# Performance work log

Hardware: AMD Instinct MI355X
Metric: run time of the kernel (lower is better)

The kernel has to match this reference:

```python
import jax, jax.numpy as jnp
import numpy as np

B, C, L = 32, 64, 4096
HIDDEN = 64
SR = 50.0
KS = (7, 15, 31, 63)
PHYS = 12
EPS_BN = 1e-5
EPS_GN = 1e-5


def _dwconv(x, w):
    # x: (B,C,L), w: (C,1,k) depthwise kernel, SAME padding for odd k
    k = w.shape[-1]
    p = (k - 1) // 2
    return jax.lax.conv_general_dilated(
        x, w, window_strides=(1,), padding=[(p, p)],
        dimension_numbers=('NCH', 'OIH', 'NCH'),
        feature_group_count=x.shape[1])


def _physics(x):
    b, c, l = x.shape
    svm = jnp.sqrt((x * x).sum(axis=1))                      # (B,L) channel norm
    svm_max = svm.max(axis=-1)
    svm_mean = svm.mean(axis=-1)
    svm_std = jnp.std(svm, axis=-1, ddof=1) + 1e-6           # torch.std is unbiased
    jerk = jnp.diff(x, axis=-1) * SR                         # (B,C,L-1)
    jerk_max = jnp.abs(jerk).max(axis=-1).mean(axis=-1)      # (B,)
    jerk_rate = jnp.diff(jerk, axis=-1) * SR
    jerk_rate_max = jnp.abs(jerk_rate).max(axis=-1).mean(axis=-1)
    sign_changes = (x[:, :, :-1] * x[:, :, 1:] < 0).astype(x.dtype)
    zcr = sign_changes.sum(axis=-1).mean(axis=-1) / l
    thr = (svm_mean + 2.0 * svm_std)[:, None]
    impact_duration = (svm > thr).astype(x.dtype).sum(axis=-1) / l
    hthr = (svm_mean + 3.0 * svm_std)[:, None]
    impact_ratio = (svm > hthr).astype(x.dtype).sum(axis=-1) / l
    free_fall = (svm < (svm_mean - svm_std)[:, None]).astype(x.dtype).sum(axis=-1) / l
    second_half = svm[:, l // 2:]
    post_stillness = jnp.tanh(1.0 / (jnp.std(second_half, axis=-1, ddof=1) + 1e-6))
    third = max(1, l // 3)
    pre_mean = svm[:, :third].mean(axis=-1)
    impact_peak = svm[:, third:2 * third].max(axis=-1)
    post_mean = svm[:, 2 * third:].mean(axis=-1)
    fall_phase = jax.nn.relu(impact_peak - pre_mean) + jax.nn.relu(impact_peak - post_mean)
    fall_phase = fall_phase / (jnp.abs(impact_peak) + 1e-6)
    spectrum = jnp.fft.rfft(x.astype(jnp.float32), axis=-1, norm='ortho')
    power = (jnp.abs(spectrum) ** 2).sum(axis=1)             # (B, L//2+1)
    freqs = jnp.linspace(0.0, 1.0, power.shape[-1], dtype=power.dtype)
    total_power = power.sum(axis=-1) + 1e-6
    spectral_centroid = (power * freqs).sum(axis=-1) / total_power
    high_freq_ratio = jnp.where(freqs > 0.4, power, 0.0).sum(axis=-1) / total_power
    feats = jnp.stack([svm_max, svm_mean, jerk_max, jerk_rate_max, zcr,
                       impact_duration, impact_ratio, post_stillness, free_fall,
                       spectral_centroid, high_freq_ratio, fall_phase], axis=-1)
    return jnp.nan_to_num(feats, nan=0.0, posinf=0.0, neginf=0.0).astype(x.dtype)


def _forward(x, dw_w7, dw_w15, dw_w31, dw_w63, bn_g, bn_b, bn_m, bn_v,
             comp_w1, comp_b1, comp_w2, comp_b2,
             pn_g, pn_b, pn_m, pn_v,
             pe_w1, pe_b1, pe_w2, pe_b2, pg_w, pg_b,
             temperature, gn_g, gn_b, proj_w, proj_b, res_scale):
    # 4 depthwise conv + BN(eval) branches
    branches = []
    for i, w in enumerate((dw_w7, dw_w15, dw_w31, dw_w63)):
        y = _dwconv(x, w)
        y = (y - bn_m[i][None, :, None]) / jnp.sqrt(bn_v[i][None, :, None] + EPS_BN) \
            * bn_g[i][None, :, None] + bn_b[i][None, :, None]
        branches.append(y)
    stacked = jnp.stack(branches, axis=1)                    # (B,4,C,L)
    # complexity net: global avg pool -> MLP
    xm = x.mean(axis=-1)                                     # (B,C)
    h = jax.nn.relu(xm @ comp_w1 + comp_b1)
    complexity_logits = h @ comp_w2 + comp_b2                # (B,4)
    # physics gate
    pf = _physics(x)                                         # (B,12)
    pf = (pf - pn_m) / jnp.sqrt(pn_v + EPS_BN) * pn_g + pn_b
    pe = jax.nn.relu(jax.nn.relu(pf @ pe_w1 + pe_b1) @ pe_w2 + pe_b2)
    physics_weights = jax.nn.sigmoid(pe @ pg_w + pg_b)       # (B,4)
    temp = jnp.maximum(temperature, 0.1)
    weights = jax.nn.softmax(complexity_logits * physics_weights / temp, axis=-1)
    mixed = jnp.einsum('bkcl,bk->bcl', stacked, weights)
    # proj: GroupNorm(1,C) -> GELU(exact) -> 1x1 conv
    mu = mixed.mean(axis=(1, 2), keepdims=True)
    var = mixed.var(axis=(1, 2), keepdims=True)
    gn = (mixed - mu) / jnp.sqrt(var + EPS_GN) * gn_g[None, :, None] + gn_b[None, :, None]
    act = jax.nn.gelu(gn, approximate=False)
    out = jnp.einsum('oc,bcl->bol', proj_w, act) + proj_b[None, :, None]
    return x + res_scale * out


def setup_inputs() -> dict:
    ks = jax.random.split(jax.random.key(0), 16)
    f32 = jnp.float32
    inp = {}
    inp['x'] = jax.random.normal(ks[0], (B, C, L), dtype=f32)
    for i, k in enumerate(KS):
        inp[f'dw_w{k}'] = jax.random.normal(ks[1 + i], (C, 1, k), dtype=f32) / np.sqrt(k)
    inp['bn_g'] = jnp.ones((4, C), f32)
    inp['bn_b'] = jnp.zeros((4, C), f32)
    inp['bn_m'] = 0.1 * jax.random.normal(ks[5], (4, C), dtype=f32)
    inp['bn_v'] = jax.random.uniform(ks[6], (4, C), dtype=f32, minval=0.5, maxval=1.5)
    inp['comp_w1'] = jax.random.normal(ks[7], (C, HIDDEN), dtype=f32) / np.sqrt(C)
    inp['comp_b1'] = jnp.zeros((HIDDEN,), f32)
    inp['comp_w2'] = jax.random.normal(ks[8], (HIDDEN, 4), dtype=f32) / np.sqrt(HIDDEN)
    inp['comp_b2'] = jnp.zeros((4,), f32)
    inp['pn_g'] = jnp.ones((PHYS,), f32)
    inp['pn_b'] = jnp.zeros((PHYS,), f32)
    inp['pn_m'] = 0.1 * jax.random.normal(ks[9], (PHYS,), dtype=f32)
    inp['pn_v'] = jax.random.uniform(ks[10], (PHYS,), dtype=f32, minval=0.5, maxval=1.5)
    inp['pe_w1'] = jax.random.normal(ks[11], (PHYS, 32), dtype=f32) / np.sqrt(PHYS)
    inp['pe_b1'] = jnp.zeros((32,), f32)
    inp['pe_w2'] = jax.random.normal(ks[12], (32, 32), dtype=f32) / np.sqrt(32)
    inp['pe_b2'] = jnp.zeros((32,), f32)
    inp['pg_w'] = jax.random.normal(ks[13], (32, 4), dtype=f32) / np.sqrt(32)
    inp['pg_b'] = jnp.zeros((4,), f32)
    inp['temperature'] = jnp.asarray(1.0, f32)
    inp['gn_g'] = jnp.ones((C,), f32)
    inp['gn_b'] = jnp.zeros((C,), f32)
    inp['proj_w'] = jax.random.normal(ks[14], (C, C), dtype=f32) / np.sqrt(C)
    inp['proj_b'] = jnp.zeros((C,), f32)
    inp['res_scale'] = jnp.asarray(0.5, f32)  # init is 0.0; 0.5 gives a non-trivial output
    return inp


def reference(x, dw_w7, dw_w15, dw_w31, dw_w63, bn_g, bn_b, bn_m, bn_v,
              comp_w1, comp_b1, comp_w2, comp_b2,
              pn_g, pn_b, pn_m, pn_v,
              pe_w1, pe_b1, pe_w2, pe_b2, pg_w, pg_b,
              temperature, gn_g, gn_b, proj_w, proj_b, res_scale):
    return _forward(x, dw_w7, dw_w15, dw_w31, dw_w63, bn_g, bn_b, bn_m, bn_v,
                    comp_w1, comp_b1, comp_w2, comp_b2, pn_g, pn_b, pn_m, pn_v,
                    pe_w1, pe_b1, pe_w2, pe_b2, pg_w, pg_b,
                    temperature, gn_g, gn_b, proj_w, proj_b, res_scale)
```

## Files before the change

kernel.cpp:

```cpp
#include <hip/hip_runtime.h>
#include <math.h>

#define LN 4096
#define CN 64
#define NTH 256

#define OFF_CHAN_SUM    0
#define OFF_CHAN_JERK   2048
#define OFF_CHAN_JRATE  4096
#define OFF_CHAN_ZCR    6144
#define OFF_SVMST_PART  8192
#define OFF_SPEC_PART   16384
#define OFF_GNP         19584
#define OFF_SVMBUF      27776

#define FP(i) ((i) + ((i) >> 4))

__device__ __forceinline__ void bfly4(float2& a, float2& b, float2& c, float2& d,
                                      float w1r, float w1i, float w2r, float w2i,
                                      float w3r, float w3i) {
  float t1r = b.x*w1r - b.y*w1i, t1i = b.x*w1i + b.y*w1r;
  float t2r = c.x*w2r - c.y*w2i, t2i = c.x*w2i + c.y*w2r;
  float t3r = d.x*w3r - d.y*w3i, t3i = d.x*w3i + d.y*w3r;
  float ar = a.x + t2r, ai = a.y + t2i;
  float br = a.x - t2r, bi = a.y - t2i;
  float cr = t1r + t3r, ci = t1i + t3i;
  float dr = t1r - t3r, di = t1i - t3i;
  a = make_float2(ar + cr, ai + ci);
  b = make_float2(br + di, bi - dr);
  c = make_float2(ar - cr, ai - ci);
  d = make_float2(br - di, bi + dr);
}

__device__ __forceinline__ float4 ldmask(const float* __restrict__ row, int idx) {
  int idxc = idx < 0 ? 0 : (idx > LN - 4 ? LN - 4 : idx);
  float4 v = *(const float4*)(row + idxc);
  float m = (idx == idxc) ? 1.f : 0.f;
  v.x *= m; v.y *= m; v.z *= m; v.w *= m;
  return v;
}

#define F16(wv,a0,a1,a2,a3,a4,a5,a6,a7,a8,a9,aA,aB,aC,aD,aE,aF) \
  acc[0]=fmaf(wv,a0,acc[0]);  acc[1]=fmaf(wv,a1,acc[1]);  acc[2]=fmaf(wv,a2,acc[2]);  acc[3]=fmaf(wv,a3,acc[3]);  \
  acc[4]=fmaf(wv,a4,acc[4]);  acc[5]=fmaf(wv,a5,acc[5]);  acc[6]=fmaf(wv,a6,acc[6]);  acc[7]=fmaf(wv,a7,acc[7]);  \
  acc[8]=fmaf(wv,a8,acc[8]);  acc[9]=fmaf(wv,a9,acc[9]);  acc[10]=fmaf(wv,aA,acc[10]); acc[11]=fmaf(wv,aB,acc[11]); \
  acc[12]=fmaf(wv,aC,acc[12]); acc[13]=fmaf(wv,aD,acc[13]); acc[14]=fmaf(wv,aE,acc[14]); acc[15]=fmaf(wv,aF,acc[15]);

__global__ __launch_bounds__(NTH) void k1_spec(const float* __restrict__ x, float* __restrict__ ws) {
  __shared__ __align__(16) char smraw[35072];
  int i = blockIdx.x;
  int b = i >> 5, sl = i & 31;
  int t = threadIdx.x;

  {
    float* tmp = (float*)smraw;
    float (*sred)[8] = (float(*)[8])(smraw + 512);
    int lt = t & 127, ch = t >> 7;
    int l = sl * 128 + lt;
    const float* xb = x + (size_t)b * CN * LN + l;
    float acc = 0.f;
#pragma unroll
    for (int cc = 0; cc < 32; cc++) {
      float v = xb[(size_t)(ch * 32 + cc) * LN];
      acc = fmaf(v, v, acc);
    }
    if (ch == 1) tmp[lt] = acc;
    __syncthreads();
    if (ch == 0) {
      acc += tmp[lt];
      float svm = sqrtf(acc);
      ws[OFF_SVMBUF + (size_t)b * LN + l] = svm;
      const int third = LN / 3;
      float vS = svm, vS2 = svm * svm;
      float vS2H  = (l >= LN/2) ? svm : 0.f;
      float vS2H2 = (l >= LN/2) ? svm * svm : 0.f;
      float vPRE  = (l < third) ? svm : 0.f;
      float vPOST = (l >= 2*third) ? svm : 0.f;
      float vMX = svm;
      float vMID = (l >= third && l < 2*third) ? svm : 0.f;
      for (int off = 32; off > 0; off >>= 1) {
        vS += __shfl_down(vS, off); vS2 += __shfl_down(vS2, off);
        vS2H += __shfl_down(vS2H, off); vS2H2 += __shfl_down(vS2H2, off);
        vPRE += __shfl_down(vPRE, off); vPOST += __shfl_down(vPOST, off);
        vMX = fmaxf(vMX, __shfl_down(vMX, off));
        vMID = fmaxf(vMID, __shfl_down(vMID, off));
      }
      if ((t & 63) == 0) {
        int w = t >> 6;
        sred[w][0]=vS; sred[w][1]=vS2; sred[w][2]=vMX; sred[w][3]=vS2H;
        sred[w][4]=vS2H2; sred[w][5]=vPRE; sred[w][6]=vMID; sred[w][7]=vPOST;
      }
    }
    __syncthreads();
    if (t == 0) {
      float* sp = ws + OFF_SVMST_PART + (size_t)(b * 32 + sl) * 8;
      sp[0]=sred[0][0]+sred[1][0];
      sp[1]=sred[0][1]+sred[1][1];
      sp[2]=fmaxf(sred[0][2],sred[1][2]);
      sp[3]=sred[0][3]+sred[1][3];
      sp[4]=sred[0][4]+sred[1][4];
      sp[5]=sred[0][5]+sred[1][5];
      sp[6]=fmaxf(sred[0][6],sred[1][6]);
      sp[7]=sred[0][7]+sred[1][7];
    }
    __syncthreads();
  }

  {
    const float* r0 = x + ((size_t)b * CN + 2 * sl) * LN;
    const float* r1 = r0 + LN;
    float2* z = (float2*)smraw;
    float (*sred8)[8] = (float(*)[8])(smraw + 34816);
    float s0 = 0.f, jm0 = 0.f, jr0 = 0.f; int zc0 = 0;
    float s1v = 0.f, jm1 = 0.f, jr1 = 0.f; int zc1 = 0;
#pragma unroll
    for (int k = 0; k < 4; k++) {
      int n4 = (k * 256 + t) * 4;
      float4 a = *(const float4*)(r0 + n4);
      float4 c = *(const float4*)(r1 + n4);
      float a4 = __shfl_down(a.x, 1), a5 = __shfl_down(a.y, 1);
      float c4 = __shfl_down(c.x, 1), c5 = __shfl_down(c.y, 1);
      if ((t & 63) == 63) {
        a4 = (n4 + 4 < LN) ? r0[n4 + 4] : 0.f;
        a5 = (n4 + 5 < LN) ? r0[n4 + 5] : 0.f;
        c4 = (n4 + 4 < LN) ? r1[n4 + 4] : 0.f;
        c5 = (n4 + 5 < LN) ? r1[n4 + 5] : 0.f;
      }
      bool nl = (n4 + 4 < LN);
      s0 += a.x + a.y + a.z + a.w;
      jm0 = fmaxf(jm0, fmaxf(fmaxf(fabsf(a.y-a.x), fabsf(a.z-a.y)), fabsf(a.w-a.z)));
      zc0 += (a.x*a.y < 0.f) + (a.y*a.z < 0.f) + (a.z*a.w < 0.f);
      jr0 = fmaxf(jr0, fmaxf(fabsf(a.z - 2.f*a.y + a.x), fabsf(a.w - 2.f*a.z + a.y)));
      if (nl) {
        jm0 = fmaxf(jm0, fabsf(a4 - a.w));
        zc0 += (a.w * a4 < 0.f);
        jr0 = fmaxf(jr0, fmaxf(fabsf(a4 - 2.f*a.w + a.z), fabsf(a5 - 2.f*a4 + a.w)));
      }
      s1v += c.x + c.y + c.z + c.w;
      jm1 = fmaxf(jm1, fmaxf(fmaxf(fabsf(c.y-c.x), fabsf(c.z-c.y)), fabsf(c.w-c.z)));
      zc1 += (c.x*c.y < 0.f) + (c.y*c.z < 0.f) + (c.z*c.w < 0.f);
      jr1 = fmaxf(jr1, fmaxf(fabsf(c.z - 2.f*c.y + c.x), fabsf(c.w - 2.f*c.z + c.y)));
      if (nl) {
        jm1 = fmaxf(jm1, fabsf(c4 - c.w));
        zc1 += (c.w * c4 < 0.f);
        jr1 = fmaxf(jr1, fmaxf(fabsf(c4 - 2.f*c.w + c.z), fabsf(c5 - 2.f*c4 + c.w)));
      }
      float ar[4] = {a.x, a.y, a.z, a.w}, crr[4] = {c.x, c.y, c.z, c.w};
#pragma unroll
      for (int q = 0; q < 4; q++) {
        unsigned n = (unsigned)(n4 + q);
        unsigned br = __brev(n) >> 20;
        unsigned dr = ((br & 0x555u) << 1) | ((br & 0xAAAu) >> 1);
        z[FP(dr)] = make_float2(ar[q], crr[q]);
      }
    }
    for (int off = 32; off > 0; off >>= 1) {
      s0 += __shfl_down(s0, off); jm0 = fmaxf(jm0, __shfl_down(jm0, off));
      jr0 = fmaxf(jr0, __shfl_down(jr0, off)); zc0 += __shfl_down(zc0, off);
      s1v += __shfl_down(s1v, off); jm1 = fmaxf(jm1, __shfl_down(jm1, off));
      jr1 = fmaxf(jr1, __shfl_down(jr1, off)); zc1 += __shfl_down(zc1, off);
    }
    if ((t & 63) == 0) {
      int w = t >> 6;
      sred8[w][0]=s0; sred8[w][1]=jm0; sred8[w][2]=jr0; sred8[w][3]=(float)zc0;
      sred8[w][4]=s1v; sred8[w][5]=jm1; sred8[w][6]=jr1; sred8[w][7]=(float)zc1;
    }
    __syncthreads();
    if (t == 0) {
      int bc0 = b * CN + 2 * sl;
      float S0=0,J0=0,JR0=0,Z0=0,S1=0,J1=0,JR1=0,Z1=0;
      for (int w = 0; w < 4; w++) {
        S0 += sred8[w][0]; J0 = fmaxf(J0, sred8[w][1]); JR0 = fmaxf(JR0, sred8[w][2]); Z0 += sred8[w][3];
        S1 += sred8[w][4]; J1 = fmaxf(J1, sred8[w][5]); JR1 = fmaxf(JR1, sred8[w][6]); Z1 += sred8[w][7];
      }
      ws[OFF_CHAN_SUM + bc0]       = S0;           ws[OFF_CHAN_SUM + bc0 + 1]   = S1;
      ws[OFF_CHAN_JERK + bc0]      = J0 * 50.f;    ws[OFF_CHAN_JERK + bc0 + 1]  = J1 * 50.f;
      ws[OFF_CHAN_JRATE + bc0]     = JR0 * 2500.f; ws[OFF_CHAN_JRATE + bc0 + 1] = JR1 * 2500.f;
      ws[OFF_CHAN_ZCR + bc0]       = Z0;           ws[OFF_CHAN_ZCR + bc0 + 1]   = Z1;
    }
    const float c8r[4] = { 1.f, 0.92387953251f, 0.70710678119f, 0.38268343236f };
    const float c8i[4] = { 0.f, -0.38268343236f, -0.70710678119f, -0.92387953251f };
#pragma unroll
    for (int p = 0; p < 3; p++) {
      const int H = (p == 0) ? 1 : (p == 1) ? 16 : 256;
      int rr = t & (H - 1);
      int B = ((t / H) * 16 * H) + rr;
      float2 E[16];
#pragma unroll
      for (int q = 0; q < 16; q++) E[q] = z[FP(B + q * H)];
      float su, cu;
      sincospif((float)rr / (8.0f * (float)H), &su, &cu);
      float ur = cu, ui = -su;
      float u2r = ur*ur - ui*ui, u2i = 2.f*ur*ui;
      float w1r = u2r*u2r - u2i*u2i, w1i = 2.f*u2r*u2i;
      float w2r = w1r*w1r - w1i*w1i, w2i = 2.f*w1r*w1i;
      float w3r = w2r*w1r - w2i*w1i, w3i = w2r*w1i + w2i*w1r;
#pragma unroll
      for (int m = 0; m < 4; m++)
        bfly4(E[4*m], E[4*m+1], E[4*m+2], E[4*m+3], w1r, w1i, w2r, w2i, w3r, w3i);
#pragma unroll
      for (int m = 0; m < 4; m++) {
        float W1r = ur*c8r[m] - ui*c8i[m];
        float W1i = ur*c8i[m] + ui*c8r[m];
        float W2r = W1r*W1r - W1i*W1i, W2i = 2.f*W1r*W1i;
        float W3r = W2r*W1r - W2i*W1i, W3i = W2r*W1i + W2i*W1r;
        bfly4(E[m], E[m+4], E[m+8], E[m+12], W1r, W1i, W2r, W2i, W3r, W3i);
      }
#pragma unroll
      for (int q = 0; q < 16; q++) z[FP(B + q * H)] = E[q];
      __syncthreads();
    }
    float tot = 0.f, cen = 0.f, hi = 0.f;
    for (int k = t; k <= LN / 2; k += NTH) {
      float p;
      if (k == 0 || k == LN / 2) {
        float2 v = z[FP(k)];
        p = v.x * v.x + v.y * v.y;
      } else {
        float2 zk = z[FP(k)], zn = z[FP(LN - k)];
        float a1 = zk.x + zn.x, a2 = zk.y - zn.y, a3 = zk.y + zn.y, a4v = zk.x - zn.x;
        p = 0.25f * (a1*a1 + a2*a2 + a3*a3 + a4v*a4v);
      }
      p *= (1.0f / LN);
      tot += p;
      cen += p * ((float)k * (1.0f / (LN / 2)));
      if (k >= 820) hi += p;
    }
    for (int off = 32; off > 0; off >>= 1) {
      tot += __shfl_down(tot, off);
      cen += __shfl_down(cen, off);
      hi  += __shfl_down(hi, off);
    }
    float (*redS)[4] = (float(*)[4])(smraw + 34816);
    if ((t & 63) == 0) { int w = t >> 6; redS[0][w] = tot; redS[1][w] = cen; redS[2][w] = hi; }
    __syncthreads();
    if (t == 0) {
      float* sp = ws + OFF_SPEC_PART + (size_t)(b * 32 + sl) * 3;
      sp[0] = redS[0][0]+redS[0][1]+redS[0][2]+redS[0][3];
      sp[1] = redS[1][0]+redS[1][1]+redS[1][2]+redS[1][3];
      sp[2] = redS[2][0]+redS[2][1]+redS[2][2]+redS[2][3];
    }
  }
}

__global__ __launch_bounds__(NTH) void k2_conv(
    const float* __restrict__ x,
    const float* __restrict__ dw7, const float* __restrict__ dw15,
    const float* __restrict__ dw31, const float* __restrict__ dw63,
    const float* __restrict__ bn_g, const float* __restrict__ bn_b,
    const float* __restrict__ bn_m, const float* __restrict__ bn_v,
    const float* __restrict__ comp_w1, const float* __restrict__ comp_b1,
    const float* __restrict__ comp_w2, const float* __restrict__ comp_b2,
    const float* __restrict__ pn_g, const float* __restrict__ pn_b,
    const float* __restrict__ pn_m, const float* __restrict__ pn_v,
    const float* __restrict__ pe_w1, const float* __restrict__ pe_b1,
    const float* __restrict__ pe_w2, const float* __restrict__ pe_b2,
    const float* __restrict__ pg_w, const float* __restrict__ pg_b,
    const float* __restrict__ temperature,
    float* __restrict__ ws, float* __restrict__ out)
{
  int i = blockIdx.x;
  int b = i >> 5, sl = i & 31;
  int t = threadIdx.x;
  __shared__ float sp8[32][8];
  __shared__ float sp3[32][3];
  __shared__ float stv[10];
  __shared__ float bc2[2];
  __shared__ float xm[64], h[64], pf[12], pe1v[32], pe2v[32], lgts[4], swts[4];
  __shared__ int ri[3][4], cnts[3];
  __shared__ float cwt[2][64];
  __shared__ float cbias[2];
  __shared__ double rda[2][4];

  if (t < 32) {
    const float* p = ws + OFF_SVMST_PART + (size_t)(b * 32 + t) * 8;
#pragma unroll
    for (int q = 0; q < 8; q++) sp8[t][q] = p[q];
  }
  if (t >= 32 && t < 64) {
    int q = t - 32;
    const float* p = ws + OFF_SPEC_PART + (size_t)(b * 32 + q) * 3;
    sp3[q][0] = p[0]; sp3[q][1] = p[1]; sp3[q][2] = p[2];
  }
  __syncthreads();
  if (t == 0) {
    float S=0,S2=0,MX=-1e30f,S2H=0,S2H2=0,PRE=0,MID=-1e30f,POST=0;
    for (int q = 0; q < 32; q++) {
      S += sp8[q][0]; S2 += sp8[q][1]; MX = fmaxf(MX, sp8[q][2]);
      S2H += sp8[q][3]; S2H2 += sp8[q][4]; PRE += sp8[q][5];
      MID = fmaxf(MID, sp8[q][6]); POST += sp8[q][7];
    }
    float tt=0,ce=0,hh=0;
    for (int q = 0; q < 32; q++) { tt += sp3[q][0]; ce += sp3[q][1]; hh += sp3[q][2]; }
    stv[0]=S; stv[1]=S2; stv[2]=MX; stv[3]=S2H; stv[4]=S2H2;
    stv[5]=PRE; stv[6]=MID; stv[7]=POST; stv[8]=ce/(tt+1e-6f); stv[9]=hh/(tt+1e-6f);
    float mean = S * (1.f / LN);
    float var = (S2 - S * S * (1.f / LN)) * (1.f / (LN - 1));
    var = fmaxf(var, 0.f);
    bc2[0] = mean;
    bc2[1] = sqrtf(var) + 1e-6f;
  }
  __syncthreads();
  float mean = bc2[0], stde = bc2[1];
  float thr2 = mean + 2.f * stde, thr3 = mean + 3.f * stde, thrf = mean - stde;
  const float* svm = ws + OFF_SVMBUF + (size_t)b * LN;
  int cc2 = 0, cc3 = 0, ccf = 0;
  for (int l = t; l < LN; l += NTH) {
    float v = svm[l];
    cc2 += (v > thr2); cc3 += (v > thr3); ccf += (v < thrf);
  }
  for (int off = 32; off > 0; off >>= 1) {
    cc2 += __shfl_down(cc2, off); cc3 += __shfl_down(cc3, off); ccf += __shfl_down(ccf, off);
  }
  {
    int w = t >> 6;
    if ((t & 63) == 0) { ri[0][w] = cc2; ri[1][w] = cc3; ri[2][w] = ccf; }
  }
  float j = 0.f, jr = 0.f, zz = 0.f;
  if (t < 64) {
    xm[t] = ws[OFF_CHAN_SUM + b * 64 + t] * (1.0f / LN);
    j  = ws[OFF_CHAN_JERK + b * 64 + t];
    jr = ws[OFF_CHAN_JRATE + b * 64 + t];
    zz = ws[OFF_CHAN_ZCR + b * 64 + t];
    for (int off = 32; off > 0; off >>= 1) {
      j += __shfl_down(j, off); jr += __shfl_down(jr, off); zz += __shfl_down(zz, off);
    }
  }
  __syncthreads();
  if (t == 0) {
    cnts[0] = ri[0][0]+ri[0][1]+ri[0][2]+ri[0][3];
    cnts[1] = ri[1][0]+ri[1][1]+ri[1][2]+ri[1][3];
    cnts[2] = ri[2][0]+ri[2][1]+ri[2][2]+ri[2][3];
    const int third = LN / 3;
    float S2H = stv[3], S2H2 = stv[4];
    float n2 = (float)(LN / 2);
    float var2 = (S2H2 - S2H * S2H / n2) / (n2 - 1.f);
    var2 = fmaxf(var2, 0.f);
    float post_still = tanhf(1.f / (sqrtf(var2) + 1e-6f));
    float pre_mean = stv[5] / (float)third;
    float post_mean = stv[7] / (float)(LN - 2 * third);
    float pk = stv[6];
    float fp2 = fmaxf(pk - pre_mean, 0.f) + fmaxf(pk - post_mean, 0.f);
    fp2 = fp2 / (fabsf(pk) + 1e-6f);
    pf[0] = stv[2];
    pf[1] = mean;
    pf[2] = j * (1.f / 64);
    pf[3] = jr * (1.f / 64);
    pf[4] = (zz * (1.f / 64)) * (1.f / LN);
    pf[5] = (float)cnts[0] / LN;
    pf[6] = (float)cnts[1] / LN;
    pf[7] = post_still;
    pf[8] = (float)cnts[2] / LN;
    pf[9] = stv[8];
    pf[10] = stv[9];
    pf[11] = fp2;
  }
  __syncthreads();
  if (t < 12) pf[t] = (pf[t] - pn_m[t]) * rsqrtf(pn_v[t] + 1e-5f) * pn_g[t] + pn_b[t];
  __syncthreads();
  if (t < 64) {
    float hv = comp_b1[t];
    for (int q = 0; q < 64; q++) hv = fmaf(xm[q], comp_w1[q * 64 + t], hv);
    h[t] = fmaxf(hv, 0.f);
  }
  if (t < 32) {
    float v = pe_b1[t];
    for (int q = 0; q < 12; q++) v = fmaf(pf[q], pe_w1[q * 32 + t], v);
    pe1v[t] = fmaxf(v, 0.f);
  }
  __syncthreads();
  if (t < 32) {
    float v = pe_b2[t];
    for (int q = 0; q < 32; q++) v = fmaf(pe1v[q], pe_w2[q * 32 + t], v);
    pe2v[t] = fmaxf(v, 0.f);
  }
  __syncthreads();
  if (t < 4) {
    float v = comp_b2[t];
    for (int q = 0; q < 64; q++) v = fmaf(h[q], comp_w2[q * 4 + t], v);
    float g = pg_b[t];
    for (int q = 0; q < 32; q++) g = fmaf(pe2v[q], pg_w[q * 4 + t], g);
    g = 1.f / (1.f + expf(-g));
    float temp = fmaxf(temperature[0], 0.1f);
    lgts[t] = v * g / temp;
  }
  __syncthreads();
  if (t < 4) {
    float m = fmaxf(fmaxf(lgts[0], lgts[1]), fmaxf(lgts[2], lgts[3]));
    float den = expf(lgts[0]-m) + expf(lgts[1]-m) + expf(lgts[2]-m) + expf(lgts[3]-m);
    swts[t] = expf(lgts[t] - m) / den;
  }
  __syncthreads();

  if (t < 128) {
    int rr = t >> 6, tau = t & 63;
    int c = 2 * sl + rr;
    float w0 = swts[0], w1 = swts[1], w2 = swts[2], w3 = swts[3];
    float sc0 = bn_g[0*64+c] * rsqrtf(bn_v[0*64+c] + 1e-5f);
    float sc1 = bn_g[1*64+c] * rsqrtf(bn_v[1*64+c] + 1e-5f);
    float sc2 = bn_g[2*64+c] * rsqrtf(bn_v[2*64+c] + 1e-5f);
    float sc3 = bn_g[3*64+c] * rsqrtf(bn_v[3*64+c] + 1e-5f);
    float a0 = w0*sc0, a1 = w1*sc1, a2 = w2*sc2, a3 = w3*sc3;
    if (tau == 0) {
      float o0 = bn_b[0*64+c] - bn_m[0*64+c] * sc0;
      float o1 = bn_b[1*64+c] - bn_m[1*64+c] * sc1;
      float o2 = bn_b[2*64+c] - bn_m[2*64+c] * sc2;
      float o3 = bn_b[3*64+c] - bn_m[3*64+c] * sc3;
      cbias[rr] = w0*o0 + w1*o1 + w2*o2 + w3*o3;
    }
    float v = 0.f;
    if (tau < 63) {
      v = a3 * dw63[c * 63 + tau];
      int i7 = tau - 28;  if (i7 >= 0 && i7 < 7)    v = fmaf(a0, dw7[c * 7 + i7], v);
      int i15 = tau - 24; if (i15 >= 0 && i15 < 15) v = fmaf(a1, dw15[c * 15 + i15], v);
      int i31 = tau - 16; if (i31 >= 0 && i31 < 31) v = fmaf(a2, dw31[c * 31 + i31], v);
    }
    cwt[rr][tau] = v;
  }
  __syncthreads();

#pragma unroll 1
  for (int r = 0; r < 2; r++) {
    int c = 2 * sl + r;
    const float* row = x + ((size_t)b * CN + c) * LN;
    const float* wtp = cwt[r];
    float bias = cbias[r];
    int l0 = t * 16, g0 = l0 - 32;
    float4 R0 = ldmask(row, g0);
    float4 R1 = ldmask(row, g0 + 4);
    float4 R2 = ldmask(row, g0 + 8);
    float4 R3 = ldmask(row, g0 + 12);
    float4 R4 = ldmask(row, g0 + 16);
    float acc[16];
#pragma unroll
    for (int jj = 0; jj < 16; jj++) acc[jj] = bias;
#pragma unroll
    for (int g = 0; g < 16; g++) {
      float w0 = wtp[4*g], w1 = wtp[4*g+1], w2 = wtp[4*g+2], w3 = wtp[4*g+3];
      F16(w0, R0.y,R0.z,R0.w,R1.x,R1.y,R1.z,R1.w,R2.x,R2.y,R2.z,R2.w,R3.x,R3.y,R3.z,R3.w,R4.x)
      F16(w1, R0.z,R0.w,R1.x,R1.y,R1.z,R1.w,R2.x,R2.y,R2.z,R2.w,R3.x,R3.y,R3.z,R3.w,R4.x,R4.y)
      F16(w2, R0.w,R1.x,R1.y,R1.z,R1.w,R2.x,R2.y,R2.z,R2.w,R3.x,R3.y,R3.z,R3.w,R4.x,R4.y,R4.z)
      F16(w3, R1.x,R1.y,R1.z,R1.w,R2.x,R2.y,R2.z,R2.w,R3.x,R3.y,R3.z,R3.w,R4.x,R4.y,R4.z,R4.w)
      if (g < 15) {
        R0 = R1; R1 = R2; R2 = R3; R3 = R4;
        R4 = ldmask(row, g0 + 4 * (g + 5));
      }
    }
    double ls = 0, ls2 = 0;
#pragma unroll
    for (int jj = 0; jj < 16; jj++) { float v = acc[jj]; ls += v; ls2 += (double)v * (double)v; }
    for (int off = 32; off > 0; off >>= 1) {
      ls += __shfl_down(ls, off);
      ls2 += __shfl_down(ls2, off);
    }
    int w = t >> 6;
    if ((t & 63) == 0) { rda[0][w] = ls; rda[1][w] = ls2; }
    float* dst = out + (size_t)(b * CN + c) * LN + l0;
#pragma unroll
    for (int q = 0; q < 4; q++) {
      float4 v4; v4.x = acc[4*q]; v4.y = acc[4*q+1]; v4.z = acc[4*q+2]; v4.w = acc[4*q+3];
      *(float4*)(dst + 4 * q) = v4;
    }
    __syncthreads();
    if (t == 0) {
      double* gp = (double*)(ws + OFF_GNP);
      gp[2 * (b * CN + c) + 0] = rda[0][0]+rda[0][1]+rda[0][2]+rda[0][3];
      gp[2 * (b * CN + c) + 1] = rda[1][0]+rda[1][1]+rda[1][2]+rda[1][3];
    }
    __syncthreads();
  }
}

__global__ __launch_bounds__(NTH) void k3_final(const float* __restrict__ x,
    const float* __restrict__ proj_w, const float* __restrict__ proj_b,
    const float* __restrict__ gn_g, const float* __restrict__ gn_b,
    const float* __restrict__ res_scale,
    const float* __restrict__ ws, float* out) {
  __shared__ __align__(16) char smraw[32840];
  int i = blockIdx.x;
  int b = i >> 5, sl = i & 31;
  int t = threadIdx.x;
  float* Wt   = (float*)smraw;
  float* actS = (float*)(smraw + 16384);
  double (*rg)[4] = (double(*)[4])(smraw + 32768);
  float* bcst = (float*)(smraw + 32832);
  const double* gp = (const double*)(ws + OFF_GNP) + (size_t)b * CN * 2;
  double g1 = 0, g2 = 0;
  if (t < CN) { g1 = gp[2*t]; g2 = gp[2*t+1]; }
  for (int off = 32; off > 0; off >>= 1) { g1 += __shfl_down(g1, off); g2 += __shfl_down(g2, off); }
  {
    int w = t >> 6;
    if ((t & 63) == 0) { rg[0][w] = g1; rg[1][w] = g2; }
  }
  for (int q = t; q < 4096; q += NTH) {
    int o = q & 63, c = q >> 6;
    Wt[c * 64 + o] = proj_w[o * 64 + c];
  }
  __syncthreads();
  if (t == 0) {
    double S1 = rg[0][0]+rg[0][1]+rg[0][2]+rg[0][3];
    double S2 = rg[1][0]+rg[1][1]+rg[1][2]+rg[1][3];
    const double NN = 64.0 * 4096.0;
    double mud = S1 / NN;
    bcst[0] = (float)mud;
    bcst[1] = rsqrtf((float)(S2 / NN - mud * mud) + 1e-5f);
  }
  __syncthreads();
  float mu = bcst[0], rstd = bcst[1];
  float rsv = res_scale[0];
  const float* mx = out + (size_t)b * CN * LN;
  const float* xb = x + (size_t)b * CN * LN;
  float* ob = out + (size_t)b * CN * LN;
#pragma unroll 1
  for (int hh = 0; hh < 2; hh++) {
    int lbase = sl * 128 + hh * 64;
    for (int q = t; q < 4096; q += NTH) {
      int c = q >> 6, l = q & 63;
      float v = mx[(size_t)c * LN + lbase + l];
      float g = (v - mu) * rstd * gn_g[c] + gn_b[c];
      actS[c * 64 + l] = 0.5f * g * (1.f + erff(g * 0.70710678118654752f));
    }
    __syncthreads();
    int lq = t & 15, og = (t >> 4) * 4;
    float4 acc4[4];
#pragma unroll
    for (int oo = 0; oo < 4; oo++) acc4[oo] = make_float4(0.f, 0.f, 0.f, 0.f);
    for (int c = 0; c < 64; c++) {
      float4 av = *(const float4*)&actS[c * 64 + lq * 4];
      float4 wv = *(const float4*)&Wt[c * 64 + og];
      float wsc[4] = {wv.x, wv.y, wv.z, wv.w};
#pragma unroll
      for (int oo = 0; oo < 4; oo++) {
        acc4[oo].x = fmaf(wsc[oo], av.x, acc4[oo].x);
        acc4[oo].y = fmaf(wsc[oo], av.y, acc4[oo].y);
        acc4[oo].z = fmaf(wsc[oo], av.z, acc4[oo].z);
        acc4[oo].w = fmaf(wsc[oo], av.w, acc4[oo].w);
      }
    }
#pragma unroll
    for (int oo = 0; oo < 4; oo++) {
      int o = og + oo;
      float pb = proj_b[o];
      size_t base = (size_t)o * LN + lbase + lq * 4;
      float4 xv = *(const float4*)&xb[base];
      float4 rr2;
      rr2.x = xv.x + rsv * (acc4[oo].x + pb);
      rr2.y = xv.y + rsv * (acc4[oo].y + pb);
      rr2.z = xv.z + rsv * (acc4[oo].z + pb);
      rr2.w = xv.w + rsv * (acc4[oo].w + pb);
      *(float4*)&ob[base] = rr2;
    }
    __syncthreads();
  }
}

extern "C" void kernel_launch(void* const* d_in, const int* in_sizes, int n_in,
                              void* d_out, int out_size, void* d_ws, size_t ws_size,
                              hipStream_t stream) {
  const float* x        = (const float*)d_in[0];
  const float* dw7      = (const float*)d_in[1];
  const float* dw15     = (const float*)d_in[2];
  const float* dw31     = (const float*)d_in[3];
  const float* dw63     = (const float*)d_in[4];
  const float* bn_g     = (const float*)d_in[5];
  const float* bn_b     = (const float*)d_in[6];
  const float* bn_m     = (const float*)d_in[7];
  const float* bn_v     = (const float*)d_in[8];
  const float* comp_w1  = (const float*)d_in[9];
  const float* comp_b1  = (const float*)d_in[10];
  const float* comp_w2  = (const float*)d_in[11];
  const float* comp_b2  = (const float*)d_in[12];
  const float* pn_g     = (const float*)d_in[13];
  const float* pn_b     = (const float*)d_in[14];
  const float* pn_m     = (const float*)d_in[15];
  const float* pn_v     = (const float*)d_in[16];
  const float* pe_w1    = (const float*)d_in[17];
  const float* pe_b1    = (const float*)d_in[18];
  const float* pe_w2    = (const float*)d_in[19];
  const float* pe_b2    = (const float*)d_in[20];
  const float* pg_w     = (const float*)d_in[21];
  const float* pg_b     = (const float*)d_in[22];
  const float* temperature = (const float*)d_in[23];
  const float* gn_g     = (const float*)d_in[24];
  const float* gn_b     = (const float*)d_in[25];
  const float* proj_w   = (const float*)d_in[26];
  const float* proj_b   = (const float*)d_in[27];
  const float* res_scale= (const float*)d_in[28];
  float* ws = (float*)d_ws;
  float* out = (float*)d_out;

  hipLaunchKernelGGL(k1_spec, dim3(1024), dim3(NTH), 0, stream, x, ws);
  hipLaunchKernelGGL(k2_conv, dim3(1024), dim3(NTH), 0, stream,
                     x, dw7, dw15, dw31, dw63, bn_g, bn_b, bn_m, bn_v,
                     comp_w1, comp_b1, comp_w2, comp_b2,
                     pn_g, pn_b, pn_m, pn_v, pe_w1, pe_b1, pe_w2, pe_b2,
                     pg_w, pg_b, temperature, ws, out);
  hipLaunchKernelGGL(k3_final, dim3(1024), dim3(NTH), 0, stream,
                     x, proj_w, proj_b, gn_g, gn_b, res_scale, ws, out);
}
```

Measured before the change: 228.7 us.

## Move per-batch gating MLP into last k1 block, slim conv kernel to one row

The per-batch statistics reduction, gating MLP and effective-kernel construction move out of every conv block into the last-arriving k1 block per batch, found with an atomic counter and threadfence. The folded conv weights and bias for each batch go to workspace. k2_conv becomes a lean kernel with one block per (batch, channel) row, 2048 blocks and a launch bound of 8. This removes work that all 1024 conv blocks repeated redundantly and raises conv parallelism. The cost is a memset launch and a serial tail in k1 where one block per batch computes 4096 weights.

```diff
diff --git a/kernel.cpp b/kernel.cpp
--- a/kernel.cpp
+++ b/kernel.cpp
@@ -13,6 +13,9 @@
 #define OFF_SPEC_PART   16384
 #define OFF_GNP         19584
 #define OFF_SVMBUF      27776
+#define OFF_CNT         158848
+#define OFF_EFF_B       158912
+#define OFF_EFF_W       160960
 
 #define FP(i) ((i) + ((i) >> 4))
 
@@ -46,8 +49,24 @@
   acc[8]=fmaf(wv,a8,acc[8]);  acc[9]=fmaf(wv,a9,acc[9]);  acc[10]=fmaf(wv,aA,acc[10]); acc[11]=fmaf(wv,aB,acc[11]); \
   acc[12]=fmaf(wv,aC,acc[12]); acc[13]=fmaf(wv,aD,acc[13]); acc[14]=fmaf(wv,aE,acc[14]); acc[15]=fmaf(wv,aF,acc[15]);
 
-__global__ __launch_bounds__(NTH) void k1_spec(const float* __restrict__ x, float* __restrict__ ws) {
+__global__ __launch_bounds__(NTH) void k1_spec(
+    const float* __restrict__ x,
+    const float* __restrict__ dw7, const float* __restrict__ dw15,
+    const float* __restrict__ dw31, const float* __restrict__ dw63,
+    const float* __restrict__ bn_g, const float* __restrict__ bn_b,
+    const float* __restrict__ bn_m, const float* __restrict__ bn_v,
+    const float* __restrict__ comp_w1, const float* __restrict__ comp_b1,
+    const float* __restrict__ comp_w2, const float* __restrict__ comp_b2,
+    const float* __restrict__ pn_g, const float* __restrict__ pn_b,
+    const float* __restrict__ pn_m, const float* __restrict__ pn_v,
+    const float* __restrict__ pe_w1, const float* __restrict__ pe_b1,
+    const float* __restrict__ pe_w2, const float* __restrict__ pe_b2,
+    const float* __restrict__ pg_w, const float* __restrict__ pg_b,
+    const float* __restrict__ temperature,
+    float* __restrict__ ws)
+{
   __shared__ __align__(16) char smraw[35072];
+  __shared__ int lastFlag;
   int i = blockIdx.x;
   int b = i >> 5, sl = i & 31;
   int t = threadIdx.x;
@@ -241,233 +260,236 @@
       sp[2] = redS[2][0]+redS[2][1]+redS[2][2]+redS[2][3];
     }
   }
-}
-
-__global__ __launch_bounds__(NTH) void k2_conv(
-    const float* __restrict__ x,
-    const float* __restrict__ dw7, const float* __restrict__ dw15,
-    const float* __restrict__ dw31, const float* __restrict__ dw63,
-    const float* __restrict__ bn_g, const float* __restrict__ bn_b,
-    const float* __restrict__ bn_m, const float* __restrict__ bn_v,
-    const float* __restrict__ comp_w1, const float* __restrict__ comp_b1,
-    const float* __restrict__ comp_w2, const float* __restrict__ comp_b2,
-    const float* __restrict__ pn_g, const float* __restrict__ pn_b,
-    const float* __restrict__ pn_m, const float* __restrict__ pn_v,
-    const float* __restrict__ pe_w1, const float* __restrict__ pe_b1,
-    const float* __restrict__ pe_w2, const float* __restrict__ pe_b2,
-    const float* __restrict__ pg_w, const float* __restrict__ pg_b,
-    const float* __restrict__ temperature,
-    float* __restrict__ ws, float* __restrict__ out)
-{
-  int i = blockIdx.x;
-  int b = i >> 5, sl = i & 31;
-  int t = threadIdx.x;
-  __shared__ float sp8[32][8];
-  __shared__ float sp3[32][3];
-  __shared__ float stv[10];
-  __shared__ float bc2[2];
-  __shared__ float xm[64], h[64], pf[12], pe1v[32], pe2v[32], lgts[4], swts[4];
-  __shared__ int ri[3][4], cnts[3];
-  __shared__ float cwt[2][64];
-  __shared__ float cbias[2];
-  __shared__ double rda[2][4];
-
-  if (t < 32) {
-    const float* p = ws + OFF_SVMST_PART + (size_t)(b * 32 + t) * 8;
-#pragma unroll
-    for (int q = 0; q < 8; q++) sp8[t][q] = p[q];
-  }
-  if (t >= 32 && t < 64) {
-    int q = t - 32;
-    const float* p = ws + OFF_SPEC_PART + (size_t)(b * 32 + q) * 3;
-    sp3[q][0] = p[0]; sp3[q][1] = p[1]; sp3[q][2] = p[2];
-  }
+
+  __threadfence();
   __syncthreads();
   if (t == 0) {
-    float S=0,S2=0,MX=-1e30f,S2H=0,S2H2=0,PRE=0,MID=-1e30f,POST=0;
-    for (int q = 0; q < 32; q++) {
-      S += sp8[q][0]; S2 += sp8[q][1]; MX = fmaxf(MX, sp8[q][2]);
-      S2H += sp8[q][3]; S2H2 += sp8[q][4]; PRE += sp8[q][5];
-      MID = fmaxf(MID, sp8[q][6]); POST += sp8[q][7];
-    }
-    float tt=0,ce=0,hh=0;
-    for (int q = 0; q < 32; q++) { tt += sp3[q][0]; ce += sp3[q][1]; hh += sp3[q][2]; }
-    stv[0]=S; stv[1]=S2; stv[2]=MX; stv[3]=S2H; stv[4]=S2H2;
-    stv[5]=PRE; stv[6]=MID; stv[7]=POST; stv[8]=ce/(tt+1e-6f); stv[9]=hh/(tt+1e-6f);
-    float mean = S * (1.f / LN);
-    float var = (S2 - S * S * (1.f / LN)) * (1.f / (LN - 1));
-    var = fmaxf(var, 0.f);
-    bc2[0] = mean;
-    bc2[1] = sqrtf(var) + 1e-6f;
+    int* cnt = (int*)(ws + OFF_CNT);
+    int old = atomicAdd(&cnt[b], 1);
+    lastFlag = (old == 31) ? 1 : 0;
   }
   __syncthreads();
-  float mean = bc2[0], stde = bc2[1];
-  float thr2 = mean + 2.f * stde, thr3 = mean + 3.f * stde, thrf = mean - stde;
-  const float* svm = ws + OFF_SVMBUF + (size_t)b * LN;
-  int cc2 = 0, cc3 = 0, ccf = 0;
-  for (int l = t; l < LN; l += NTH) {
-    float v = svm[l];
-    cc2 += (v > thr2); cc3 += (v > thr3); ccf += (v < thrf);
-  }
+  if (!lastFlag) return;
+  __threadfence();
+
+  {
+    float (*sp8)[8] = (float(*)[8])smraw;
+    float (*sp3)[3] = (float(*)[3])(smraw + 1024);
+    float* stv  = (float*)(smraw + 1408);
+    float* bc2  = (float*)(smraw + 1448);
+    float* xm   = (float*)(smraw + 1456);
+    float* hG   = (float*)(smraw + 1712);
+    float* pf   = (float*)(smraw + 1968);
+    float* pe1v = (float*)(smraw + 2016);
+    float* pe2v = (float*)(smraw + 2144);
+    float* lgts = (float*)(smraw + 2272);
+    float* swts = (float*)(smraw + 2288);
+    int (*ri)[4] = (int(*)[4])(smraw + 2304);
+    int* cnts   = (int*)(smraw + 2352);
+    __syncthreads();
+
+    if (t < 32) {
+      const float* p = ws + OFF_SVMST_PART + (size_t)(b * 32 + t) * 8;
+#pragma unroll
+      for (int q = 0; q < 8; q++) sp8[t][q] = p[q];
+    }
+    if (t >= 32 && t < 64) {
+      int q = t - 32;
+      const float* p = ws + OFF_SPEC_PART + (size_t)(b * 32 + q) * 3;
+      sp3[q][0] = p[0]; sp3[q][1] = p[1]; sp3[q][2] = p[2];
+    }
+    __syncthreads();
+    if (t == 0) {
+      float S=0,S2=0,MX=-1e30f,S2H=0,S2H2=0,PRE=0,MID=-1e30f,POST=0;
+      for (int q = 0; q < 32; q++) {
+        S += sp8[q][0]; S2 += sp8[q][1]; MX = fmaxf(MX, sp8[q][2]);
+        S2H += sp8[q][3]; S2H2 += sp8[q][4]; PRE += sp8[q][5];
+        MID = fmaxf(MID, sp8[q][6]); POST += sp8[q][7];
+      }
+      float tt=0,ce=0,hh=0;
+      for (int q = 0; q < 32; q++) { tt += sp3[q][0]; ce += sp3[q][1]; hh += sp3[q][2]; }
+      stv[0]=S; stv[1]=S2; stv[2]=MX; stv[3]=S2H; stv[4]=S2H2;
+      stv[5]=PRE; stv[6]=MID; stv[7]=POST; stv[8]=ce/(tt+1e-6f); stv[9]=hh/(tt+1e-6f);
+      float mean = S * (1.f / LN);
+      float var = (S2 - S * S * (1.f / LN)) * (1.f / (LN - 1));
+      var = fmaxf(var, 0.f);
+      bc2[0] = mean;
+      bc2[1] = sqrtf(var) + 1e-6f;
+    }
+    __syncthreads();
+    float mean = bc2[0], stde = bc2[1];
+    float thr2 = mean + 2.f * stde, thr3 = mean + 3.f * stde, thrf = mean - stde;
+    const float* svm = ws + OFF_SVMBUF + (size_t)b * LN;
+    int cc2 = 0, cc3 = 0, ccf = 0;
+    for (int l = t; l < LN; l += NTH) {
+      float v = svm[l];
+      cc2 += (v > thr2); cc3 += (v > thr3); ccf += (v < thrf);
+    }
+    for (int off = 32; off > 0; off >>= 1) {
+      cc2 += __shfl_down(cc2, off); cc3 += __shfl_down(cc3, off); ccf += __shfl_down(ccf, off);
+    }
+    {
+      int w = t >> 6;
+      if ((t & 63) == 0) { ri[0][w] = cc2; ri[1][w] = cc3; ri[2][w] = ccf; }
+    }
+    float j = 0.f, jr = 0.f, zz = 0.f;
+    if (t < 64) {
+      xm[t] = ws[OFF_CHAN_SUM + b * 64 + t] * (1.0f / LN);
+      j  = ws[OFF_CHAN_JERK + b * 64 + t];
+      jr = ws[OFF_CHAN_JRATE + b * 64 + t];
+      zz = ws[OFF_CHAN_ZCR + b * 64 + t];
+      for (int off = 32; off > 0; off >>= 1) {
+        j += __shfl_down(j, off); jr += __shfl_down(jr, off); zz += __shfl_down(zz, off);
+      }
+    }
+    __syncthreads();
+    if (t == 0) {
+      cnts[0] = ri[0][0]+ri[0][1]+ri[0][2]+ri[0][3];
+      cnts[1] = ri[1][0]+ri[1][1]+ri[1][2]+ri[1][3];
+      cnts[2] = ri[2][0]+ri[2][1]+ri[2][2]+ri[2][3];
+      const int third = LN / 3;
+      float S2H = stv[3], S2H2 = stv[4];
+      float n2 = (float)(LN / 2);
+      float var2 = (S2H2 - S2H * S2H / n2) / (n2 - 1.f);
+      var2 = fmaxf(var2, 0.f);
+      float post_still = tanhf(1.f / (sqrtf(var2) + 1e-6f));
+      float pre_mean = stv[5] / (float)third;
+      float post_mean = stv[7] / (float)(LN - 2 * third);
+      float pk = stv[6];
+      float fp2 = fmaxf(pk - pre_mean, 0.f) + fmaxf(pk - post_mean, 0.f);
+      fp2 = fp2 / (fabsf(pk) + 1e-6f);
+      pf[0] = stv[2];
+      pf[1] = mean;
+      pf[2] = j * (1.f / 64);
+      pf[3] = jr * (1.f / 64);
+      pf[4] = (zz * (1.f / 64)) * (1.f / LN);
+      pf[5] = (float)cnts[0] / LN;
+      pf[6] = (float)cnts[1] / LN;
+      pf[7] = post_still;
+      pf[8] = (float)cnts[2] / LN;
+      pf[9] = stv[8];
+      pf[10] = stv[9];
+      pf[11] = fp2;
+    }
+    __syncthreads();
+    if (t < 12) pf[t] = (pf[t] - pn_m[t]) * rsqrtf(pn_v[t] + 1e-5f) * pn_g[t] + pn_b[t];
+    __syncthreads();
+    if (t < 64) {
+      float hv = comp_b1[t];
+      for (int q = 0; q < 64; q++) hv = fmaf(xm[q], comp_w1[q * 64 + t], hv);
+      hG[t] = fmaxf(hv, 0.f);
+    }
+    if (t < 32) {
+      float v = pe_b1[t];
+      for (int q = 0; q < 12; q++) v = fmaf(pf[q], pe_w1[q * 32 + t], v);
+      pe1v[t] = fmaxf(v, 0.f);
+    }
+    __syncthreads();
+    if (t < 32) {
+      float v = pe_b2[t];
+      for (int q = 0; q < 32; q++) v = fmaf(pe1v[q], pe_w2[q * 32 + t], v);
+      pe2v[t] = fmaxf(v, 0.f);
+    }
+    __syncthreads();
+    if (t < 4) {
+      float v = comp_b2[t];
+      for (int q = 0; q < 64; q++) v = fmaf(hG[q], comp_w2[q * 4 + t], v);
+      float g = pg_b[t];
+      for (int q = 0; q < 32; q++) g = fmaf(pe2v[q], pg_w[q * 4 + t], g);
+      g = 1.f / (1.f + expf(-g));
+      float temp = fmaxf(temperature[0], 0.1f);
+      lgts[t] = v * g / temp;
+    }
+    __syncthreads();
+    if (t < 4) {
+      float m = fmaxf(fmaxf(lgts[0], lgts[1]), fmaxf(lgts[2], lgts[3]));
+      float den = expf(lgts[0]-m) + expf(lgts[1]-m) + expf(lgts[2]-m) + expf(lgts[3]-m);
+      swts[t] = expf(lgts[t] - m) / den;
+    }
+    __syncthreads();
+
+    float w0 = swts[0], w1 = swts[1], w2 = swts[2], w3 = swts[3];
+    for (int idx = t; idx < 64 * 64; idx += NTH) {
+      int c = idx >> 6, tau = idx & 63;
+      float sc0 = bn_g[0*64+c] * rsqrtf(bn_v[0*64+c] + 1e-5f);
+      float sc1 = bn_g[1*64+c] * rsqrtf(bn_v[1*64+c] + 1e-5f);
+      float sc2 = bn_g[2*64+c] * rsqrtf(bn_v[2*64+c] + 1e-5f);
+      float sc3 = bn_g[3*64+c] * rsqrtf(bn_v[3*64+c] + 1e-5f);
+      float a0 = w0*sc0, a1 = w1*sc1, a2 = w2*sc2, a3 = w3*sc3;
+      if (tau == 0) {
+        float o0 = bn_b[0*64+c] - bn_m[0*64+c] * sc0;
+        float o1 = bn_b[1*64+c] - bn_m[1*64+c] * sc1;
+        float o2 = bn_b[2*64+c] - bn_m[2*64+c] * sc2;
+        float o3 = bn_b[3*64+c] - bn_m[3*64+c] * sc3;
+        ws[OFF_EFF_B + b * 64 + c] = w0*o0 + w1*o1 + w2*o2 + w3*o3;
+      }
+      float v = 0.f;
+      if (tau < 63) {
+        v = a3 * dw63[c * 63 + tau];
+        int i7 = tau - 28;  if (i7 >= 0 && i7 < 7)    v = fmaf(a0, dw7[c * 7 + i7], v);
+        int i15 = tau - 24; if (i15 >= 0 && i15 < 15) v = fmaf(a1, dw15[c * 15 + i15], v);
+        int i31 = tau - 16; if (i31 >= 0 && i31 < 31) v = fmaf(a2, dw31[c * 31 + i31], v);
+      }
+      ws[OFF_EFF_W + ((size_t)b * 64 + c) * 64 + tau] = v;
+    }
+  }
+}
+
+__global__ __launch_bounds__(NTH, 8) void k2_conv(const float* __restrict__ x,
+                                                  float* __restrict__ ws,
+                                                  float* __restrict__ out) {
+  int bc = blockIdx.x;
+  int t = threadIdx.x;
+  __shared__ float wt[64];
+  __shared__ float biasS;
+  __shared__ double rda[2][4];
+  if (t < 64) wt[t] = ws[OFF_EFF_W + (size_t)bc * 64 + t];
+  if (t == 0) biasS = ws[OFF_EFF_B + bc];
+  const float* row = x + (size_t)bc * LN;
+  int l0 = t * 16;
+  int g0 = l0 - 32;
+  float4 R0 = ldmask(row, g0);
+  float4 R1 = ldmask(row, g0 + 4);
+  float4 R2 = ldmask(row, g0 + 8);
+  float4 R3 = ldmask(row, g0 + 12);
+  float4 R4 = ldmask(row, g0 + 16);
+  __syncthreads();
+  float bias = biasS;
+  float acc[16];
+#pragma unroll
+  for (int jj = 0; jj < 16; jj++) acc[jj] = bias;
+#pragma unroll
+  for (int g = 0; g < 16; g++) {
+    float w0 = wt[4*g], w1 = wt[4*g+1], w2 = wt[4*g+2], w3 = wt[4*g+3];
+    F16(w0, R0.y,R0.z,R0.w,R1.x,R1.y,R1.z,R1.w,R2.x,R2.y,R2.z,R2.w,R3.x,R3.y,R3.z,R3.w,R4.x)
+    F16(w1, R0.z,R0.w,R1.x,R1.y,R1.z,R1.w,R2.x,R2.y,R2.z,R2.w,R3.x,R3.y,R3.z,R3.w,R4.x,R4.y)
+    F16(w2, R0.w,R1.x,R1.y,R1.z,R1.w,R2.x,R2.y,R2.z,R2.w,R3.x,R3.y,R3.z,R3.w,R4.x,R4.y,R4.z)
+    F16(w3, R1.x,R1.y,R1.z,R1.w,R2.x,R2.y,R2.z,R2.w,R3.x,R3.y,R3.z,R3.w,R4.x,R4.y,R4.z,R4.w)
+    if (g < 15) {
+      R0 = R1; R1 = R2; R2 = R3; R3 = R4;
+      R4 = ldmask(row, g0 + 4 * (g + 5));
+    }
+  }
+  double ls = 0, ls2 = 0;
+#pragma unroll
+  for (int jj = 0; jj < 16; jj++) { float v = acc[jj]; ls += v; ls2 += (double)v * (double)v; }
   for (int off = 32; off > 0; off >>= 1) {
-    cc2 += __shfl_down(cc2, off); cc3 += __shfl_down(cc3, off); ccf += __shfl_down(ccf, off);
-  }
-  {
-    int w = t >> 6;
-    if ((t & 63) == 0) { ri[0][w] = cc2; ri[1][w] = cc3; ri[2][w] = ccf; }
-  }
-  float j = 0.f, jr = 0.f, zz = 0.f;
-  if (t < 64) {
-    xm[t] = ws[OFF_CHAN_SUM + b * 64 + t] * (1.0f / LN);
-    j  = ws[OFF_CHAN_JERK + b * 64 + t];
-    jr = ws[OFF_CHAN_JRATE + b * 64 + t];
-    zz = ws[OFF_CHAN_ZCR + b * 64 + t];
-    for (int off = 32; off > 0; off >>= 1) {
-      j += __shfl_down(j, off); jr += __shfl_down(jr, off); zz += __shfl_down(zz, off);
-    }
-  }
+    ls += __shfl_down(ls, off);
+    ls2 += __shfl_down(ls2, off);
+  }
+  int w = t >> 6;
+  if ((t & 63) == 0) { rda[0][w] = ls; rda[1][w] = ls2; }
   __syncthreads();
   if (t == 0) {
-    cnts[0] = ri[0][0]+ri[0][1]+ri[0][2]+ri[0][3];
-    cnts[1] = ri[1][0]+ri[1][1]+ri[1][2]+ri[1][3];
-    cnts[2] = ri[2][0]+ri[2][1]+ri[2][2]+ri[2][3];
-    const int third = LN / 3;
-    float S2H = stv[3], S2H2 = stv[4];
-    float n2 = (float)(LN / 2);
-    float var2 = (S2H2 - S2H * S2H / n2) / (n2 - 1.f);
-    var2 = fmaxf(var2, 0.f);
-    float post_still = tanhf(1.f / (sqrtf(var2) + 1e-6f));
-    float pre_mean = stv[5] / (float)third;
-    float post_mean = stv[7] / (float)(LN - 2 * third);
-    float pk = stv[6];
-    float fp2 = fmaxf(pk - pre_mean, 0.f) + fmaxf(pk - post_mean, 0.f);
-    fp2 = fp2 / (fabsf(pk) + 1e-6f);
-    pf[0] = stv[2];
-    pf[1] = mean;
-    pf[2] = j * (1.f / 64);
-    pf[3] = jr * (1.f / 64);
-    pf[4] = (zz * (1.f / 64)) * (1.f / LN);
-    pf[5] = (float)cnts[0] / LN;
-    pf[6] = (float)cnts[1] / LN;
-    pf[7] = post_still;
-    pf[8] = (float)cnts[2] / LN;
-    pf[9] = stv[8];
-    pf[10] = stv[9];
-    pf[11] = fp2;
-  }
-  __syncthreads();
-  if (t < 12) pf[t] = (pf[t] - pn_m[t]) * rsqrtf(pn_v[t] + 1e-5f) * pn_g[t] + pn_b[t];
-  __syncthreads();
-  if (t < 64) {
-    float hv = comp_b1[t];
-    for (int q = 0; q < 64; q++) hv = fmaf(xm[q], comp_w1[q * 64 + t], hv);
-    h[t] = fmaxf(hv, 0.f);
-  }
-  if (t < 32) {
-    float v = pe_b1[t];
-    for (int q = 0; q < 12; q++) v = fmaf(pf[q], pe_w1[q * 32 + t], v);
-    pe1v[t] = fmaxf(v, 0.f);
-  }
-  __syncthreads();
-  if (t < 32) {
-    float v = pe_b2[t];
-    for (int q = 0; q < 32; q++) v = fmaf(pe1v[q], pe_w2[q * 32 + t], v);
-    pe2v[t] = fmaxf(v, 0.f);
-  }
-  __syncthreads();
-  if (t < 4) {
-    float v = comp_b2[t];
-    for (int q = 0; q < 64; q++) v = fmaf(h[q], comp_w2[q * 4 + t], v);
-    float g = pg_b[t];
-    for (int q = 0; q < 32; q++) g = fmaf(pe2v[q], pg_w[q * 4 + t], g);
-    g = 1.f / (1.f + expf(-g));
-    float temp = fmaxf(temperature[0], 0.1f);
-    lgts[t] = v * g / temp;
-  }
-  __syncthreads();
-  if (t < 4) {
-    float m = fmaxf(fmaxf(lgts[0], lgts[1]), fmaxf(lgts[2], lgts[3]));
-    float den = expf(lgts[0]-m) + expf(lgts[1]-m) + expf(lgts[2]-m) + expf(lgts[3]-m);
-    swts[t] = expf(lgts[t] - m) / den;
-  }
-  __syncthreads();
-
-  if (t < 128) {
-    int rr = t >> 6, tau = t & 63;
-    int c = 2 * sl + rr;
-    float w0 = swts[0], w1 = swts[1], w2 = swts[2], w3 = swts[3];
-    float sc0 = bn_g[0*64+c] * rsqrtf(bn_v[0*64+c] + 1e-5f);
-    float sc1 = bn_g[1*64+c] * rsqrtf(bn_v[1*64+c] + 1e-5f);
-    float sc2 = bn_g[2*64+c] * rsqrtf(bn_v[2*64+c] + 1e-5f);
-    float sc3 = bn_g[3*64+c] * rsqrtf(bn_v[3*64+c] + 1e-5f);
-    float a0 = w0*sc0, a1 = w1*sc1, a2 = w2*sc2, a3 = w3*sc3;
-    if (tau == 0) {
-      float o0 = bn_b[0*64+c] - bn_m[0*64+c] * sc0;
-      float o1 = bn_b[1*64+c] - bn_m[1*64+c] * sc1;
-      float o2 = bn_b[2*64+c] - bn_m[2*64+c] * sc2;
-      float o3 = bn_b[3*64+c] - bn_m[3*64+c] * sc3;
-      cbias[rr] = w0*o0 + w1*o1 + w2*o2 + w3*o3;
-    }
-    float v = 0.f;
-    if (tau < 63) {
-      v = a3 * dw63[c * 63 + tau];
-      int i7 = tau - 28;  if (i7 >= 0 && i7 < 7)    v = fmaf(a0, dw7[c * 7 + i7], v);
-      int i15 = tau - 24; if (i15 >= 0 && i15 < 15) v = fmaf(a1, dw15[c * 15 + i15], v);
-      int i31 = tau - 16; if (i31 >= 0 && i31 < 31) v = fmaf(a2, dw31[c * 31 + i31], v);
-    }
-    cwt[rr][tau] = v;
-  }
-  __syncthreads();
-
-#pragma unroll 1
-  for (int r = 0; r < 2; r++) {
-    int c = 2 * sl + r;
-    const float* row = x + ((size_t)b * CN + c) * LN;
-    const float* wtp = cwt[r];
-    float bias = cbias[r];
-    int l0 = t * 16, g0 = l0 - 32;
-    float4 R0 = ldmask(row, g0);
-    float4 R1 = ldmask(row, g0 + 4);
-    float4 R2 = ldmask(row, g0 + 8);
-    float4 R3 = ldmask(row, g0 + 12);
-    float4 R4 = ldmask(row, g0 + 16);
-    float acc[16];
-#pragma unroll
-    for (int jj = 0; jj < 16; jj++) acc[jj] = bias;
-#pragma unroll
-    for (int g = 0; g < 16; g++) {
-      float w0 = wtp[4*g], w1 = wtp[4*g+1], w2 = wtp[4*g+2], w3 = wtp[4*g+3];
-      F16(w0, R0.y,R0.z,R0.w,R1.x,R1.y,R1.z,R1.w,R2.x,R2.y,R2.z,R2.w,R3.x,R3.y,R3.z,R3.w,R4.x)
-      F16(w1, R0.z,R0.w,R1.x,R1.y,R1.z,R1.w,R2.x,R2.y,R2.z,R2.w,R3.x,R3.y,R3.z,R3.w,R4.x,R4.y)
-      F16(w2, R0.w,R1.x,R1.y,R1.z,R1.w,R2.x,R2.y,R2.z,R2.w,R3.x,R3.y,R3.z,R3.w,R4.x,R4.y,R4.z)
-      F16(w3, R1.x,R1.y,R1.z,R1.w,R2.x,R2.y,R2.z,R2.w,R3.x,R3.y,R3.z,R3.w,R4.x,R4.y,R4.z,R4.w)
-      if (g < 15) {
-        R0 = R1; R1 = R2; R2 = R3; R3 = R4;
-        R4 = ldmask(row, g0 + 4 * (g + 5));
-      }
-    }
-    double ls = 0, ls2 = 0;
-#pragma unroll
-    for (int jj = 0; jj < 16; jj++) { float v = acc[jj]; ls += v; ls2 += (double)v * (double)v; }
-    for (int off = 32; off > 0; off >>= 1) {
-      ls += __shfl_down(ls, off);
-      ls2 += __shfl_down(ls2, off);
-    }
-    int w = t >> 6;
-    if ((t & 63) == 0) { rda[0][w] = ls; rda[1][w] = ls2; }
-    float* dst = out + (size_t)(b * CN + c) * LN + l0;
-#pragma unroll
-    for (int q = 0; q < 4; q++) {
-      float4 v4; v4.x = acc[4*q]; v4.y = acc[4*q+1]; v4.z = acc[4*q+2]; v4.w = acc[4*q+3];
-      *(float4*)(dst + 4 * q) = v4;
-    }
-    __syncthreads();
-    if (t == 0) {
-      double* gp = (double*)(ws + OFF_GNP);
-      gp[2 * (b * CN + c) + 0] = rda[0][0]+rda[0][1]+rda[0][2]+rda[0][3];
-      gp[2 * (b * CN + c) + 1] = rda[1][0]+rda[1][1]+rda[1][2]+rda[1][3];
-    }
-    __syncthreads();
+    double* gp = (double*)(ws + OFF_GNP);
+    gp[2 * bc + 0] = rda[0][0]+rda[0][1]+rda[0][2]+rda[0][3];
+    gp[2 * bc + 1] = rda[1][0]+rda[1][1]+rda[1][2]+rda[1][3];
+  }
+  float* dst = out + (size_t)bc * LN + l0;
+#pragma unroll
+  for (int q = 0; q < 4; q++) {
+    float4 v; v.x = acc[4*q]; v.y = acc[4*q+1]; v.z = acc[4*q+2]; v.w = acc[4*q+3];
+    *(float4*)(dst + 4 * q) = v;
   }
 }
 
@@ -589,12 +611,14 @@
   float* ws = (float*)d_ws;
   float* out = (float*)d_out;
 
-  hipLaunchKernelGGL(k1_spec, dim3(1024), dim3(NTH), 0, stream, x, ws);
-  hipLaunchKernelGGL(k2_conv, dim3(1024), dim3(NTH), 0, stream,
+  hipMemsetAsync(ws + OFF_CNT, 0, 32 * sizeof(int), stream);
+
+  hipLaunchKernelGGL(k1_spec, dim3(1024), dim3(NTH), 0, stream,
                      x, dw7, dw15, dw31, dw63, bn_g, bn_b, bn_m, bn_v,
                      comp_w1, comp_b1, comp_w2, comp_b2,
                      pn_g, pn_b, pn_m, pn_v, pe_w1, pe_b1, pe_w2, pe_b2,
-                     pg_w, pg_b, temperature, ws, out);
+                     pg_w, pg_b, temperature, ws);
+  hipLaunchKernelGGL(k2_conv, dim3(2048), dim3(NTH), 0, stream, x, ws, out);
   hipLaunchKernelGGL(k3_final, dim3(1024), dim3(NTH), 0, stream,
                      x, proj_w, proj_b, gn_g, gn_b, res_scale, ws, out);
 }
```

Measured after the change: 361.1 us. +57.9%, slower.
